# Kernel optimization log

Hardware: AMD Instinct MI355X
Metric: run time of the kernel (lower is better)

Reference implementation:

```python
import jax, jax.numpy as jnp
import numpy as np

B, C, IMG, P = 16, 3, 224, 16
HP = IMG // P          # 14
NP = HP * HP           # 196 patches
PD = C * P * P         # 768 patch_dim
DIM, OUT = 768, 1024
DI, NS, DC, DTR = 2 * DIM, 16, 4, 48  # mamba: d_inner, d_state, d_conv, dt_rank
NL = 2


def _ln(x, g, b, eps=1e-5):
    m = x.mean(-1, keepdims=True)
    v = ((x - m) ** 2).mean(-1, keepdims=True)
    return (x - m) / jnp.sqrt(v + eps) * g + b


def _gelu(x):
    return jax.nn.gelu(x, approximate=False)


def _mamba_block(x, in_w, in_b, conv_w, conv_b, xproj_w, dt_w, dt_b, Alog, D, out_w, out_b):
    # x: [B, L, DIM]
    Bb, L, _ = x.shape
    xr = x @ in_w + in_b                      # [B, L, 2*DI]
    xi, res = jnp.split(xr, 2, axis=-1)
    # causal depthwise conv1d over L
    xp = jnp.pad(xi, ((0, 0), (DC - 1, 0), (0, 0)))
    xc = conv_b + sum(xp[:, k:k + L, :] * conv_w[:, k] for k in range(DC))
    xi = jax.nn.silu(xc)
    dbc = xi @ xproj_w                        # [B, L, DTR + 2*NS]
    delta = jax.nn.softplus(dbc[..., :DTR] @ dt_w + dt_b)   # [B, L, DI]
    Bm = dbc[..., DTR:DTR + NS]               # [B, L, NS]
    Cm = dbc[..., DTR + NS:]                  # [B, L, NS]
    A = -jnp.exp(Alog)                        # [DI, NS]
    dA = jnp.exp(delta[..., None] * A)                       # [B, L, DI, NS]
    dBu = delta[..., None] * Bm[:, :, None, :] * xi[..., None]

    def step(h, inp):
        dA_t, dBu_t, C_t = inp
        h = dA_t * h + dBu_t                  # [B, DI, NS]
        y = jnp.einsum('bdn,bn->bd', h, C_t)
        return h, y

    h0 = jnp.zeros((Bb, DI, NS), x.dtype)
    _, ys = jax.lax.scan(step, h0, (dA.transpose(1, 0, 2, 3),
                                    dBu.transpose(1, 0, 2, 3),
                                    Cm.transpose(1, 0, 2)))
    y = ys.transpose(1, 0, 2) + D * xi        # [B, L, DI]
    y = y * jax.nn.silu(res)
    return y @ out_w + out_b


def setup_inputs() -> dict:
    key = jax.random.key(0)
    ks = iter(jax.random.split(key, 40))

    def rn(shape, s=0.02):
        return jax.random.normal(next(ks), shape, jnp.float32) * s

    inp = {
        'img': jax.random.normal(next(ks), (B, C, IMG, IMG), jnp.float32),
        'sa_w': rn((1, 2, 7, 7), 0.1),
        'pe_w': rn((PD, DIM)), 'pe_b': jnp.zeros((DIM,), jnp.float32),
        'pos_emb': rn((1, NP, DIM), 1.0),
        'm_in_w': rn((NL, DIM, 2 * DI)), 'm_in_b': jnp.zeros((NL, 2 * DI), jnp.float32),
        'm_conv_w': rn((NL, DI, DC), 0.1), 'm_conv_b': jnp.zeros((NL, DI), jnp.float32),
        'm_xproj_w': rn((NL, DI, DTR + 2 * NS)),
        'm_dt_w': rn((NL, DTR, DI)), 'm_dt_b': rn((NL, DI), 0.01),
        'm_Alog': jnp.tile(jnp.log(jnp.arange(1, NS + 1, dtype=jnp.float32))[None, None, :], (NL, DI, 1)),
        'm_D': jnp.ones((NL, DI), jnp.float32),
        'm_out_w': rn((NL, DI, DIM)), 'm_out_b': jnp.zeros((NL, DIM), jnp.float32),
        'em_w': rn((DIM, OUT)), 'em_b': jnp.zeros((OUT,), jnp.float32),
        'em_g': jnp.ones((OUT,), jnp.float32), 'em_bt': jnp.zeros((OUT,), jnp.float32),
        'att_w': rn((OUT, OUT)), 'att_b': jnp.zeros((OUT,), jnp.float32),
        'att_g': jnp.ones((OUT,), jnp.float32), 'att_bt': jnp.zeros((OUT,), jnp.float32),
        'lat_g': jnp.ones((OUT,), jnp.float32), 'lat_bt': jnp.zeros((OUT,), jnp.float32),
    }
    return inp


def reference(img, sa_w, pe_w, pe_b, pos_emb,
              m_in_w, m_in_b, m_conv_w, m_conv_b, m_xproj_w,
              m_dt_w, m_dt_b, m_Alog, m_D, m_out_w, m_out_b,
              em_w, em_b, em_g, em_bt, att_w, att_b, att_g, att_bt,
              lat_g, lat_bt):
    # spatial attention gate
    avg = img.mean(axis=1, keepdims=True)
    mx = img.max(axis=1, keepdims=True)
    a = jnp.concatenate([avg, mx], axis=1)                    # [B,2,H,W]
    a = jax.lax.conv_general_dilated(a, sa_w, (1, 1), [(3, 3), (3, 3)],
                                     dimension_numbers=('NCHW', 'OIHW', 'NCHW'))
    img = img * jax.nn.sigmoid(a)
    # patchify: b c (h p1)(w p2) -> b (h w) (p1 p2 c)
    x = img.reshape(B, C, HP, P, HP, P).transpose(0, 2, 4, 3, 5, 1).reshape(B, NP, PD)
    x = x @ pe_w + pe_b                                       # [B, NP, DIM]
    x = x + pos_emb[:, :NP]
    for i in range(NL):
        x = _mamba_block(x, m_in_w[i], m_in_b[i], m_conv_w[i], m_conv_b[i],
                         m_xproj_w[i], m_dt_w[i], m_dt_b[i], m_Alog[i], m_D[i],
                         m_out_w[i], m_out_b[i])
    y = _gelu(_ln(x @ em_w + em_b, em_g, em_bt))              # [B, NP, OUT]
    z = jax.nn.softmax(_gelu(_ln(y @ att_w + att_b, att_g, att_bt)), axis=1)
    pooled = (y * z).sum(axis=1)                              # [B, OUT]
    return _ln(pooled, lat_g, lat_bt)
```

## Files before the change

### kernel.cpp

```cpp
#include <hip/hip_runtime.h>
#include <math.h>

static constexpr int NB = 16;
static constexpr int NC = 3;
static constexpr int IM = 224;
static constexpr int IMP = IM * IM;
static constexpr int HPq = 14;
static constexpr int NPq = 196;
static constexpr int OUTq = 1024;
static constexpr int DIq = 1536;
static constexpr int ROWS = NB * NPq;
static constexpr int MPAD = 3200;

typedef __bf16 bf8_t __attribute__((ext_vector_type(8)));
typedef float f4_t __attribute__((ext_vector_type(4)));
typedef unsigned short us8 __attribute__((ext_vector_type(8)));
typedef const __attribute__((address_space(1))) unsigned int cgu32;
typedef __attribute__((address_space(3))) unsigned int lu32;

__device__ inline unsigned short f2bf(float x) {
    unsigned u = __builtin_bit_cast(unsigned, x);
    unsigned r = (u + 0x7FFFu + ((u >> 16) & 1u)) >> 16;
    return (unsigned short)r;
}
__device__ inline float bf2f(unsigned short v) {
    return __builtin_bit_cast(float, (unsigned)v << 16);
}
__device__ inline float fast_sig(float x) {
    return __builtin_amdgcn_rcpf(1.f + __expf(-x));
}
__device__ inline float fast_softplus(float v) {
    return fmaxf(v, 0.f) + __logf(1.f + __expf(-fabsf(v)));
}

template<int CTRL>
__device__ inline float dpp_add(float x) {
    int v = __builtin_amdgcn_update_dpp(0, __builtin_bit_cast(int, x), CTRL, 0xF, 0xF, true);
    return x + __builtin_bit_cast(float, v);
}

__global__ __launch_bounds__(256) void k_avgmax(const float* __restrict__ img, float* __restrict__ am) {
    int idx = blockIdx.x * 256 + threadIdx.x;
    if (idx >= NB * IMP / 4) return;
    int p4 = (idx % (IMP / 4)) * 4, b = idx / (IMP / 4);
    const float* ib = img + (size_t)b * NC * IMP + p4;
    float4 c0 = *(const float4*)ib;
    float4 c1 = *(const float4*)(ib + IMP);
    float4 c2 = *(const float4*)(ib + 2 * IMP);
    float4 av, mx;
    av.x = (c0.x + c1.x + c2.x) * (1.f / 3.f); mx.x = fmaxf(c0.x, fmaxf(c1.x, c2.x));
    av.y = (c0.y + c1.y + c2.y) * (1.f / 3.f); mx.y = fmaxf(c0.y, fmaxf(c1.y, c2.y));
    av.z = (c0.z + c1.z + c2.z) * (1.f / 3.f); mx.z = fmaxf(c0.z, fmaxf(c1.z, c2.z));
    av.w = (c0.w + c1.w + c2.w) * (1.f / 3.f); mx.w = fmaxf(c0.w, fmaxf(c1.w, c2.w));
    *(float4*)(am + (size_t)(b * 2 + 0) * IMP + p4) = av;
    *(float4*)(am + (size_t)(b * 2 + 1) * IMP + p4) = mx;
}

__global__ __launch_bounds__(256) void k_gatepatch(const float* __restrict__ img, const float* __restrict__ am,
                                                   const float* __restrict__ saw, unsigned short* __restrict__ G) {
    int quad = blockIdx.x * 256 + threadIdx.x;
    if (quad >= NB * IMP / 4) return;
    int pq = quad % (IMP / 4), b = quad / (IMP / 4);
    int x0 = (pq % 56) * 4;
    int y = pq / 56;
    float acc0 = 0.f, acc1 = 0.f, acc2 = 0.f, acc3 = 0.f;
    const bool lok = (x0 >= 4), rok = (x0 <= IM - 8);
    #pragma unroll
    for (int ci = 0; ci < 2; ci++) {
        const float* amc = am + (size_t)(b * 2 + ci) * IMP;
        const float* wc = saw + ci * 49;
        #pragma unroll
        for (int kh = 0; kh < 7; kh++) {
            int yy = y + kh - 3;
            if (yy < 0 || yy >= IM) continue;
            const float* rowp = amc + yy * IM;
            float4 lv = lok ? *(const float4*)(rowp + x0 - 4) : make_float4(0.f, 0.f, 0.f, 0.f);
            float4 mv = *(const float4*)(rowp + x0);
            float4 rv = rok ? *(const float4*)(rowp + x0 + 4) : make_float4(0.f, 0.f, 0.f, 0.f);
            float f[12] = {lv.x, lv.y, lv.z, lv.w, mv.x, mv.y, mv.z, mv.w, rv.x, rv.y, rv.z, rv.w};
            #pragma unroll
            for (int kw = 0; kw < 7; kw++) {
                float w = wc[kh * 7 + kw];
                acc0 = fmaf(w, f[kw + 1], acc0);
                acc1 = fmaf(w, f[kw + 2], acc1);
                acc2 = fmaf(w, f[kw + 3], acc2);
                acc3 = fmaf(w, f[kw + 4], acc3);
            }
        }
    }
    float s0 = fast_sig(acc0), s1 = fast_sig(acc1), s2 = fast_sig(acc2), s3 = fast_sig(acc3);
    const float* ib = img + (size_t)b * NC * IMP + y * IM + x0;
    float4 c0 = *(const float4*)ib;
    float4 c1 = *(const float4*)(ib + IMP);
    float4 c2 = *(const float4*)(ib + 2 * IMP);
    int hy = y >> 4, py = y & 15, hx = x0 >> 4, px0 = x0 & 15;
    size_t base = ((size_t)(b * NPq + hy * HPq + hx) * 768) + (size_t)(py * 16 + px0) * 3;
    ushort4 o0, o1, o2;
    o0.x = f2bf(c0.x * s0); o0.y = f2bf(c1.x * s0); o0.z = f2bf(c2.x * s0);
    o0.w = f2bf(c0.y * s1);
    o1.x = f2bf(c1.y * s1); o1.y = f2bf(c2.y * s1);
    o1.z = f2bf(c0.z * s2); o1.w = f2bf(c1.z * s2);
    o2.x = f2bf(c2.z * s2);
    o2.y = f2bf(c0.w * s3); o2.z = f2bf(c1.w * s3); o2.w = f2bf(c2.w * s3);
    *(ushort4*)(G + base + 0) = o0;
    *(ushort4*)(G + base + 4) = o1;
    *(ushort4*)(G + base + 8) = o2;
}

__global__ __launch_bounds__(256) void k_transpose_all(const float* pe_w, const float* in_w, const float* ot_w,
                                                       const float* em_w, const float* at_w,
                                                       unsigned short* wpe, unsigned short* win0, unsigned short* win1,
                                                       unsigned short* wot0, unsigned short* wot1,
                                                       unsigned short* wem, unsigned short* wat) {
    int bid = blockIdx.x;
    const float* W; unsigned short* Wt; int K, N, local;
    if (bid < 576)       { W = pe_w; Wt = wpe; K = 768; N = 768; local = bid; }
    else if (bid < 2880) { W = in_w; Wt = win0; K = 768; N = 3072; local = bid - 576; }
    else if (bid < 5184) { W = in_w + (size_t)768 * 3072; Wt = win1; K = 768; N = 3072; local = bid - 2880; }
    else if (bid < 6336) { W = ot_w; Wt = wot0; K = 1536; N = 768; local = bid - 5184; }
    else if (bid < 7488) { W = ot_w + (size_t)1536 * 768; Wt = wot1; K = 1536; N = 768; local = bid - 6336; }
    else if (bid < 8256) { W = em_w; Wt = wem; K = 768; N = 1024; local = bid - 7488; }
    else                 { W = at_w; Wt = wat; K = 1024; N = 1024; local = bid - 8256; }
    int gx = N / 32;
    int n0 = (local % gx) * 32, k0 = (local / gx) * 32;
    __shared__ float t[32][33];
    int c = threadIdx.x & 31, r8 = threadIdx.x >> 5;
    #pragma unroll
    for (int i = 0; i < 4; i++) {
        int r = r8 + i * 8;
        t[r][c] = W[(size_t)(k0 + r) * N + n0 + c];
    }
    __syncthreads();
    #pragma unroll
    for (int i = 0; i < 4; i++) {
        int r = r8 + i * 8;
        Wt[(size_t)(n0 + r) * K + k0 + c] = f2bf(t[c][r]);
    }
}

enum { EPI_NONE = 0, EPI_POSEMB = 1 };

template<int EPI, bool CBF>
__global__ __launch_bounds__(256) void k_gemm_bf(const unsigned short* __restrict__ A,
                                                 const unsigned short* __restrict__ Wt,
                                                 const float* __restrict__ bias,
                                                 void* __restrict__ Cv, int ldc,
                                                 int M, int N, int K,
                                                 const float* __restrict__ extra) {
    constexpr int BM = 128, BN = 64;
    __shared__ __align__(16) unsigned short As[2][BM * 64];
    __shared__ __align__(16) unsigned short Bs[2][BN * 64];
    const int bm = blockIdx.y * BM, bn = blockIdx.x * BN;
    const int tid = threadIdx.x;
    const int lane = tid & 63;
    const int wbase = tid & ~63;
    const int wr = ((tid >> 7) & 1) * 64;
    const int wc = ((tid >> 6) & 1) * 32;
    const int lr = lane & 15, lq = lane >> 4;

    f4_t acc[4][2] = {};

    auto stage = [&](int buf, int k0) {
        #pragma unroll
        for (int i = 0; i < 4; i++) {
            int gid2 = i * 256 + tid;
            int r = gid2 >> 3, g = gid2 & 7;
            const unsigned short* src = A + (size_t)(bm + r) * K + k0 + ((g ^ (r & 7)) * 8);
            __builtin_amdgcn_global_load_lds((cgu32*)src,
                (lu32*)&As[buf][(i * 256 + wbase) * 8], 16, 0, 0);
        }
        #pragma unroll
        for (int i = 0; i < 2; i++) {
            int gid2 = i * 256 + tid;
            int r = gid2 >> 3, g = gid2 & 7;
            const unsigned short* src = Wt + (size_t)(bn + r) * K + k0 + ((g ^ (r & 7)) * 8);
            __builtin_amdgcn_global_load_lds((cgu32*)src,
                (lu32*)&Bs[buf][(i * 256 + wbase) * 8], 16, 0, 0);
        }
    };

    stage(0, 0);
    __syncthreads();
    int cur = 0;
    for (int k0 = 0; k0 < K; k0 += 64) {
        if (k0 + 64 < K) stage(cur ^ 1, k0 + 64);
        #pragma unroll
        for (int h = 0; h < 2; h++) {
            bf8_t af[4], bfr[2];
            #pragma unroll
            for (int mb = 0; mb < 4; mb++) {
                int row = wr + mb * 16 + lr;
                int g = h * 4 + lq;
                af[mb] = *(const bf8_t*)&As[cur][row * 64 + ((g ^ (row & 7)) * 8)];
            }
            #pragma unroll
            for (int nb = 0; nb < 2; nb++) {
                int rn = wc + nb * 16 + lr;
                int g = h * 4 + lq;
                bfr[nb] = *(const bf8_t*)&Bs[cur][rn * 64 + ((g ^ (rn & 7)) * 8)];
            }
            #pragma unroll
            for (int mb = 0; mb < 4; mb++)
                #pragma unroll
                for (int nb = 0; nb < 2; nb++)
                    acc[mb][nb] = __builtin_amdgcn_mfma_f32_16x16x32_bf16(af[mb], bfr[nb], acc[mb][nb], 0, 0, 0);
        }
        __syncthreads();
        cur ^= 1;
    }

    #pragma unroll
    for (int mb = 0; mb < 4; mb++) {
        #pragma unroll
        for (int nb = 0; nb < 2; nb++) {
            int col = bn + wc + nb * 16 + lr;
            #pragma unroll
            for (int q = 0; q < 4; q++) {
                int row = bm + wr + mb * 16 + lq * 4 + q;
                if (row < M) {
                    float v = acc[mb][nb][q];
                    if (bias) v += bias[col];
                    if (EPI == EPI_POSEMB) v += extra[(size_t)(row % NPq) * N + col];
                    if (CBF) ((unsigned short*)Cv)[(size_t)row * ldc + col] = f2bf(v);
                    else     ((float*)Cv)[(size_t)row * ldc + col] = v;
                }
            }
        }
    }
}

__global__ __launch_bounds__(256) void k_gemm_bf2(const unsigned short* __restrict__ A,
                                                  const unsigned short* __restrict__ Wt,
                                                  const float* __restrict__ bias,
                                                  unsigned short* __restrict__ xr2,
                                                  unsigned short* __restrict__ sres,
                                                  int M, int K) {
    constexpr int BM = 128;
    __shared__ __align__(16) unsigned short As[BM * 64];
    __shared__ __align__(16) unsigned short Bs[BM * 64];
    const int bm = blockIdx.y * BM, bn = blockIdx.x * BM;
    const int tid = threadIdx.x;
    const int lane = tid & 63;
    const int wbase = tid & ~63;
    const int wid = tid >> 6;
    const int wr = (wid >> 1) * 64;
    const int wc = (wid & 1) * 64;
    const int lr = lane & 15, lq = lane >> 4;

    f4_t acc[4][4] = {};

    for (int k0 = 0; k0 < K; k0 += 64) {
        #pragma unroll
        for (int i = 0; i < 4; i++) {
            int gid2 = i * 256 + tid;
            int r = gid2 >> 3, g = gid2 & 7;
            const unsigned short* srcA = A + (size_t)(bm + r) * K + k0 + ((g ^ (r & 7)) * 8);
            __builtin_amdgcn_global_load_lds((cgu32*)srcA,
                (lu32*)&As[(i * 256 + wbase) * 8], 16, 0, 0);
            const unsigned short* srcB = Wt + (size_t)(bn + r) * K + k0 + ((g ^ (r & 7)) * 8);
            __builtin_amdgcn_global_load_lds((cgu32*)srcB,
                (lu32*)&Bs[(i * 256 + wbase) * 8], 16, 0, 0);
        }
        __syncthreads();
        #pragma unroll
        for (int h = 0; h < 2; h++) {
            bf8_t af[4], bfr[4];
            #pragma unroll
            for (int mb = 0; mb < 4; mb++) {
                int row = wr + mb * 16 + lr;
                int g = h * 4 + lq;
                af[mb] = *(const bf8_t*)&As[row * 64 + ((g ^ (row & 7)) * 8)];
            }
            #pragma unroll
            for (int nb = 0; nb < 4; nb++) {
                int rn = wc + nb * 16 + lr;
                int g = h * 4 + lq;
                bfr[nb] = *(const bf8_t*)&Bs[rn * 64 + ((g ^ (rn & 7)) * 8)];
            }
            #pragma unroll
            for (int mb = 0; mb < 4; mb++)
                #pragma unroll
                for (int nb = 0; nb < 4; nb++)
                    acc[mb][nb] = __builtin_amdgcn_mfma_f32_16x16x32_bf16(af[mb], bfr[nb], acc[mb][nb], 0, 0, 0);
        }
        __syncthreads();
    }

    #pragma unroll
    for (int mb = 0; mb < 4; mb++) {
        #pragma unroll
        for (int nb = 0; nb < 4; nb++) {
            int col = bn + wc + nb * 16 + lr;
            float bv = bias[col];
            #pragma unroll
            for (int q = 0; q < 4; q++) {
                int row = bm + wr + mb * 16 + lq * 4 + q;
                if (row < M) {
                    float v = acc[mb][nb][q] + bv;
                    if (col < DIq) xr2[(size_t)row * DIq + col] = f2bf(v);
                    else           sres[(size_t)row * DIq + (col - DIq)] = f2bf(v * fast_sig(v));
                }
            }
        }
    }
}

static constexpr int XP_KS = 8;
static constexpr int XP_KC = 1536 / XP_KS;

__global__ __launch_bounds__(256) void k_xproj_part(const unsigned short* __restrict__ xi2b,
                                                    const float* __restrict__ W,
                                                    float* __restrict__ part) {
    __shared__ float As[32][65];
    __shared__ __align__(16) float Bs[64][80];
    int m0 = blockIdx.x * 32;
    int kc0 = blockIdx.y * XP_KC;
    int tid = threadIdx.x;
    int row = tid >> 3, cg = (tid & 7) * 10;
    float acc[10] = {};
    for (int k0 = 0; k0 < XP_KC; k0 += 64) {
        {
            int r = tid >> 3, c8 = (tid & 7) * 8;
            us8 v = *(const us8*)(xi2b + (size_t)(m0 + r) * 1536 + kc0 + k0 + c8);
            #pragma unroll
            for (int j = 0; j < 8; j++) As[r][c8 + j] = bf2f(v[j]);
        }
        #pragma unroll
        for (int i = 0; i < 5; i++) {
            int id = tid + i * 256;
            int r = id / 20, c4 = (id % 20) * 4;
            *(float4*)&Bs[r][c4] = *(const float4*)(W + (size_t)(kc0 + k0 + r) * 80 + c4);
        }
        __syncthreads();
        #pragma unroll
        for (int kk = 0; kk < 64; kk++) {
            float a = As[row][kk];
            #pragma unroll
            for (int j = 0; j < 10; j++)
                acc[j] = fmaf(a, Bs[kk][cg + j], acc[j]);
        }
        __syncthreads();
    }
    float* p = part + ((size_t)blockIdx.y * ROWS + m0 + row) * 80 + cg;
    #pragma unroll
    for (int j = 0; j < 10; j++) p[j] = acc[j];
}

static constexpr int DT_RPB = 4;
__global__ __launch_bounds__(384) void k_dtred(const float* __restrict__ part, const float* __restrict__ W,
                                               const float* __restrict__ bias, float* __restrict__ de,
                                               float* __restrict__ dbc) {
    int r0 = blockIdx.x * DT_RPB;
    int tid = threadIdx.x;
    __shared__ float ds[DT_RPB][80];
    if (tid < DT_RPB * 80) {
        int row = tid / 80, col = tid % 80;
        const int S = ROWS * 80;
        const float* p = part + (size_t)(r0 + row) * 80 + col;
        float s = 0.f;
        #pragma unroll
        for (int k = 0; k < XP_KS; k++) s += p[(size_t)k * S];
        ds[row][col] = s;
        if (col >= 48) dbc[(size_t)(r0 + row) * 80 + col] = s;
    }
    __syncthreads();
    int j = tid * 4;
    float4 b = *(const float4*)(bias + j);
    float4 a0 = b, a1 = b, a2 = b, a3 = b;
    for (int k = 0; k < 48; k++) {
        float4 w = *(const float4*)(W + (size_t)k * 1536 + j);
        float d0 = ds[0][k], d1 = ds[1][k], d2 = ds[2][k], d3 = ds[3][k];
        a0.x = fmaf(d0, w.x, a0.x); a0.y = fmaf(d0, w.y, a0.y); a0.z = fmaf(d0, w.z, a0.z); a0.w = fmaf(d0, w.w, a0.w);
        a1.x = fmaf(d1, w.x, a1.x); a1.y = fmaf(d1, w.y, a1.y); a1.z = fmaf(d1, w.z, a1.z); a1.w = fmaf(d1, w.w, a1.w);
        a2.x = fmaf(d2, w.x, a2.x); a2.y = fmaf(d2, w.y, a2.y); a2.z = fmaf(d2, w.z, a2.z); a2.w = fmaf(d2, w.w, a2.w);
        a3.x = fmaf(d3, w.x, a3.x); a3.y = fmaf(d3, w.y, a3.y); a3.z = fmaf(d3, w.z, a3.z); a3.w = fmaf(d3, w.w, a3.w);
    }
    float4 o;
    o.x = fast_softplus(a0.x); o.y = fast_softplus(a0.y); o.z = fast_softplus(a0.z); o.w = fast_softplus(a0.w);
    *(float4*)(de + (size_t)(r0 + 0) * 1536 + j) = o;
    o.x = fast_softplus(a1.x); o.y = fast_softplus(a1.y); o.z = fast_softplus(a1.z); o.w = fast_softplus(a1.w);
    *(float4*)(de + (size_t)(r0 + 1) * 1536 + j) = o;
    o.x = fast_softplus(a2.x); o.y = fast_softplus(a2.y); o.z = fast_softplus(a2.z); o.w = fast_softplus(a2.w);
    *(float4*)(de + (size_t)(r0 + 2) * 1536 + j) = o;
    o.x = fast_softplus(a3.x); o.y = fast_softplus(a3.y); o.z = fast_softplus(a3.z); o.w = fast_softplus(a3.w);
    *(float4*)(de + (size_t)(r0 + 3) * 1536 + j) = o;
}

__global__ __launch_bounds__(256) void k_conv_silu(const unsigned short* __restrict__ xr2, const float* __restrict__ cw,
                                                   const float* __restrict__ cb, unsigned short* __restrict__ xi2b) {
    int idx4 = blockIdx.x * 256 + threadIdx.x;
    if (idx4 >= ROWS * DIq / 4) return;
    int d4 = (idx4 % (DIq / 4)) * 4;
    int bt = idx4 / (DIq / 4);
    int t = bt % NPq, b = bt / NPq;
    const unsigned short* base = xr2 + (size_t)b * NPq * DIq + d4;
    float4 s = *(const float4*)(cb + d4);
    float4 w0 = *(const float4*)(cw + (d4 + 0) * 4);
    float4 w1 = *(const float4*)(cw + (d4 + 1) * 4);
    float4 w2 = *(const float4*)(cw + (d4 + 2) * 4);
    float4 w3 = *(const float4*)(cw + (d4 + 3) * 4);
    if (t >= 3) {
        ushort4 v = *(const ushort4*)(base + (size_t)(t - 3) * DIq);
        s.x = fmaf(bf2f(v.x), w0.x, s.x); s.y = fmaf(bf2f(v.y), w1.x, s.y);
        s.z = fmaf(bf2f(v.z), w2.x, s.z); s.w = fmaf(bf2f(v.w), w3.x, s.w);
    }
    if (t >= 2) {
        ushort4 v = *(const ushort4*)(base + (size_t)(t - 2) * DIq);
        s.x = fmaf(bf2f(v.x), w0.y, s.x); s.y = fmaf(bf2f(v.y), w1.y, s.y);
        s.z = fmaf(bf2f(v.z), w2.y, s.z); s.w = fmaf(bf2f(v.w), w3.y, s.w);
    }
    if (t >= 1) {
        ushort4 v = *(const ushort4*)(base + (size_t)(t - 1) * DIq);
        s.x = fmaf(bf2f(v.x), w0.z, s.x); s.y = fmaf(bf2f(v.y), w1.z, s.y);
        s.z = fmaf(bf2f(v.z), w2.z, s.z); s.w = fmaf(bf2f(v.w), w3.z, s.w);
    }
    {
        ushort4 v = *(const ushort4*)(base + (size_t)t * DIq);
        s.x = fmaf(bf2f(v.x), w0.w, s.x); s.y = fmaf(bf2f(v.y), w1.w, s.y);
        s.z = fmaf(bf2f(v.z), w2.w, s.z); s.w = fmaf(bf2f(v.w), w3.w, s.w);
    }
    ushort4 xo;
    xo.x = f2bf(s.x * fast_sig(s.x)); xo.y = f2bf(s.y * fast_sig(s.y));
    xo.z = f2bf(s.z * fast_sig(s.z)); xo.w = f2bf(s.w * fast_sig(s.w));
    *(ushort4*)(xi2b + (size_t)bt * DIq + d4) = xo;
}

static constexpr int STB = 28;

__global__ __launch_bounds__(256) void k_scan(const float* __restrict__ delta, const unsigned short* __restrict__ xi2b,
                                              const float* __restrict__ dbc, const unsigned short* __restrict__ sresb,
                                              const float* __restrict__ Alog, const float* __restrict__ Dv,
                                              unsigned short* __restrict__ ys) {
    const int b = blockIdx.x;
    const int d0 = blockIdx.y * 32;
    const int tid = threadIdx.x;
    const int dl = tid >> 3;
    const int np = tid & 7;
    const int d = d0 + dl;
    const float A0 = -__expf(Alog[d * 16 + np]);
    const float A1 = -__expf(Alog[d * 16 + np + 8]);
    const float Dd = Dv[d];
    const int tr = tid >> 5;
    const int dls = tid & 31;

    __shared__ float2 sdu[2][STB][32];
    __shared__ float sbc[2][STB][32];

    const float* gde = delta + ((size_t)b * NPq + tr) * DIq + d0 + dls;
    const unsigned short* gu  = xi2b  + ((size_t)b * NPq + tr) * DIq + d0 + dls;
    const unsigned short* gsr = sresb + ((size_t)b * NPq + tr) * DIq + d0 + dls;
    const float* gbc = dbc + ((size_t)b * NPq + tr) * 80 + 48 + dls;
    unsigned short* gy = ys + (size_t)b * NPq * DIq + d;

    float rde[4], rbc[4];
    unsigned short ruu[4], rss[4];

    auto stageLoad = [&](int c) {
        const int t0 = c * STB;
        #pragma unroll
        for (int j = 0; j < 3; j++) {
            int off = (t0 + 8 * j) * DIq;
            rde[j] = gde[off];
            ruu[j] = gu[off];
            rss[j] = gsr[off];
            rbc[j] = gbc[(t0 + 8 * j) * 80];
        }
        if (tid < 128) {
            int off = (t0 + 24) * DIq;
            rde[3] = gde[off];
            ruu[3] = gu[off];
            rss[3] = gsr[off];
            rbc[3] = gbc[(t0 + 24) * 80];
        }
    };
    auto stageWrite = [&](int buf) {
        const int pi = (dls & 7) * 4 + (dls >> 3);
        #pragma unroll
        for (int j = 0; j < 3; j++) {
            int t = tr + 8 * j;
            unsigned pk = ((unsigned)ruu[j] << 16) | rss[j];
            sdu[buf][t][dls] = make_float2(rde[j], __builtin_bit_cast(float, pk));
            sbc[buf][t][pi] = rbc[j];
        }
        if (tid < 128) {
            int t = tr + 24;
            unsigned pk = ((unsigned)ruu[3] << 16) | rss[3];
            sdu[buf][t][dls] = make_float2(rde[3], __builtin_bit_cast(float, pk));
            sbc[buf][t][pi] = rbc[3];
        }
    };

    stageLoad(0);
    stageWrite(0);
    __syncthreads();

    float h0 = 0.f, h1 = 0.f;
    int cur = 0;
    for (int c = 0; c < 7; c++) {
        if (c < 6) stageLoad(c + 1);
        #pragma unroll 4
        for (int t = 0; t < STB; t++) {
            float2 duv = sdu[cur][t][dl];
            float4 bc = *(const float4*)&sbc[cur][t][np * 4];
            unsigned bits = __builtin_bit_cast(unsigned, duv.y);
            float u  = __builtin_bit_cast(float, bits & 0xFFFF0000u);
            float sr = __builtin_bit_cast(float, bits << 16);
            float a0 = __expf(duv.x * A0), a1 = __expf(duv.x * A1);
            float deu = duv.x * u;
            h0 = fmaf(a0, h0, deu * bc.x);
            h1 = fmaf(a1, h1, deu * bc.y);
            float p = fmaf(h1, bc.w, h0 * bc.z);
            p = dpp_add<0xB1>(p);
            p = dpp_add<0x4E>(p);
            p = dpp_add<0x141>(p);
            if (np == 0) gy[(size_t)(c * STB + t) * DIq] = f2bf(fmaf(Dd, u, p) * sr);
        }
        if (c < 6) stageWrite(cur ^ 1);
        __syncthreads();
        cur ^= 1;
    }
}

template<bool OBF>
__global__ __launch_bounds__(256) void k_ln_gelu(const float* __restrict__ in, const float* __restrict__ g,
                                                 const float* __restrict__ bt, void* __restrict__ outv) {
    int row = blockIdx.x;
    const float* x = in + (size_t)row * OUTq;
    float4 v = ((const float4*)x)[threadIdx.x];
    float s = v.x + v.y + v.z + v.w;
    float ss = v.x * v.x + v.y * v.y + v.z * v.z + v.w * v.w;
    #pragma unroll
    for (int off = 32; off >= 1; off >>= 1) { s += __shfl_down(s, off); ss += __shfl_down(ss, off); }
    __shared__ float sh[10];
    int wid = threadIdx.x >> 6, lid = threadIdx.x & 63;
    if (lid == 0) { sh[wid] = s; sh[4 + wid] = ss; }
    __syncthreads();
    if (threadIdx.x == 0) {
        float S = sh[0] + sh[1] + sh[2] + sh[3], SS = sh[4] + sh[5] + sh[6] + sh[7];
        float m = S * (1.f / OUTq);
        float var = SS * (1.f / OUTq) - m * m;
        sh[8] = m; sh[9] = rsqrtf(var + 1e-5f);
    }
    __syncthreads();
    float m = sh[8], rst = sh[9];
    float4 gv = ((const float4*)g)[threadIdx.x];
    float4 bv = ((const float4*)bt)[threadIdx.x];
    float4 o;
    float y0 = (v.x - m) * rst * gv.x + bv.x; o.x = 0.5f * y0 * (1.f + erff(y0 * 0.70710678118f));
    float y1 = (v.y - m) * rst * gv.y + bv.y; o.y = 0.5f * y1 * (1.f + erff(y1 * 0.70710678118f));
    float y2 = (v.z - m) * rst * gv.z + bv.z; o.z = 0.5f * y2 * (1.f + erff(y2 * 0.70710678118f));
    float y3 = (v.w - m) * rst * gv.w + bv.w; o.w = 0.5f * y3 * (1.f + erff(y3 * 0.70710678118f));
    if (OBF) {
        ushort4 o4;
        o4.x = f2bf(o.x); o4.y = f2bf(o.y); o4.z = f2bf(o.z); o4.w = f2bf(o.w);
        ((ushort4*)((unsigned short*)outv + (size_t)row * OUTq))[threadIdx.x] = o4;
    } else {
        ((float4*)((float*)outv + (size_t)row * OUTq))[threadIdx.x] = o;
    }
}

__global__ __launch_bounds__(256) void k_softpool(const float* __restrict__ gm, const unsigned short* __restrict__ ym,
                                                  float* __restrict__ pooled) {
    int b = blockIdx.y;
    int jl = threadIdx.x & 63;
    int j = blockIdx.x * 64 + jl;
    int tc = threadIdx.x >> 6;
    const float* gb = gm + (size_t)b * NPq * OUTq + j;
    const unsigned short* yb = ym + (size_t)b * NPq * OUTq + j;
    int t0 = tc * 49;
    float m = -1e30f, s = 0.f, ps = 0.f;
    for (int t = t0; t < t0 + 49; t++) {
        float g = gb[(size_t)t * OUTq];
        float y = bf2f(yb[(size_t)t * OUTq]);
        float mn = fmaxf(m, g);
        float sc = __expf(m - mn);
        float e = __expf(g - mn);
        s = fmaf(s, sc, e);
        ps = fmaf(ps, sc, y * e);
        m = mn;
    }
    __shared__ float sm[4][64], ssum[4][64], sps[4][64];
    sm[tc][jl] = m; ssum[tc][jl] = s; sps[tc][jl] = ps;
    __syncthreads();
    if (tc == 0) {
        float m0 = sm[0][jl], m1 = sm[1][jl], m2 = sm[2][jl], m3 = sm[3][jl];
        float mt = fmaxf(fmaxf(m0, m1), fmaxf(m2, m3));
        float e0 = __expf(m0 - mt), e1 = __expf(m1 - mt);
        float e2 = __expf(m2 - mt), e3 = __expf(m3 - mt);
        float st = ssum[0][jl] * e0 + ssum[1][jl] * e1 + ssum[2][jl] * e2 + ssum[3][jl] * e3;
        float pt = sps[0][jl] * e0 + sps[1][jl] * e1 + sps[2][jl] * e2 + sps[3][jl] * e3;
        pooled[b * OUTq + j] = pt / st;
    }
}

__global__ __launch_bounds__(256) void k_final_ln(const float* __restrict__ p, const float* __restrict__ g,
                                                  const float* __restrict__ bt, float* __restrict__ out) {
    int row = blockIdx.x;
    const float* x = p + (size_t)row * OUTq;
    float4 v = ((const float4*)x)[threadIdx.x];
    float s = v.x + v.y + v.z + v.w;
    float ss = v.x * v.x + v.y * v.y + v.z * v.z + v.w * v.w;
    #pragma unroll
    for (int off = 32; off >= 1; off >>= 1) { s += __shfl_down(s, off); ss += __shfl_down(ss, off); }
    __shared__ float sh[10];
    int wid = threadIdx.x >> 6, lid = threadIdx.x & 63;
    if (lid == 0) { sh[wid] = s; sh[4 + wid] = ss; }
    __syncthreads();
    if (threadIdx.x == 0) {
        float S = sh[0] + sh[1] + sh[2] + sh[3], SS = sh[4] + sh[5] + sh[6] + sh[7];
        float m = S * (1.f / OUTq);
        float var = SS * (1.f / OUTq) - m * m;
        sh[8] = m; sh[9] = rsqrtf(var + 1e-5f);
    }
    __syncthreads();
    float m = sh[8], rst = sh[9];
    float4 gv = ((const float4*)g)[threadIdx.x];
    float4 bv = ((const float4*)bt)[threadIdx.x];
    float4 o;
    o.x = (v.x - m) * rst * gv.x + bv.x;
    o.y = (v.y - m) * rst * gv.y + bv.y;
    o.z = (v.z - m) * rst * gv.z + bv.z;
    o.w = (v.w - m) * rst * gv.w + bv.w;
    ((float4*)(out + (size_t)row * OUTq))[threadIdx.x] = o;
}

extern "C" void kernel_launch(void* const* d_in, const int* in_sizes, int n_in,
                              void* d_out, int out_size, void* d_ws, size_t ws_size,
                              hipStream_t stream) {
    const float* img   = (const float*)d_in[0];
    const float* sa_w  = (const float*)d_in[1];
    const float* pe_w  = (const float*)d_in[2];
    const float* pe_b  = (const float*)d_in[3];
    const float* pos   = (const float*)d_in[4];
    const float* in_w  = (const float*)d_in[5];
    const float* in_b  = (const float*)d_in[6];
    const float* cv_w  = (const float*)d_in[7];
    const float* cv_b  = (const float*)d_in[8];
    const float* xp_w  = (const float*)d_in[9];
    const float* dt_w  = (const float*)d_in[10];
    const float* dt_b  = (const float*)d_in[11];
    const float* Alog  = (const float*)d_in[12];
    const float* Dv    = (const float*)d_in[13];
    const float* ot_w  = (const float*)d_in[14];
    const float* ot_b  = (const float*)d_in[15];
    const float* em_w  = (const float*)d_in[16];
    const float* em_b  = (const float*)d_in[17];
    const float* em_g  = (const float*)d_in[18];
    const float* em_bt = (const float*)d_in[19];
    const float* at_w  = (const float*)d_in[20];
    const float* at_b  = (const float*)d_in[21];
    const float* at_g  = (const float*)d_in[22];
    const float* at_bt = (const float*)d_in[23];
    const float* la_g  = (const float*)d_in[24];
    const float* la_bt = (const float*)d_in[25];

    char* ws = (char*)d_ws;
    auto al = [](size_t x) { return (x + 255) & ~(size_t)255; };
    size_t SZ_am   = (size_t)NB * 2 * IMP * 4;
    size_t SZ_G    = (size_t)MPAD * 768 * 2;
    size_t SZ_x    = (size_t)MPAD * 768 * 2;
    size_t SZ_xr2  = (size_t)ROWS * DIq * 2;
    size_t SZ_xi2  = (size_t)ROWS * DIq * 2;
    size_t SZ_de   = (size_t)ROWS * DIq * 4;
    size_t SZ_dbc  = (size_t)ROWS * 80 * 4;
    size_t SZ_ys   = (size_t)MPAD * DIq * 2;
    size_t SZ_sres = (size_t)ROWS * DIq * 2;
    size_t SZ_yem  = (size_t)MPAD * 1024 * 2;
    size_t SZ_pool = (size_t)NB * OUTq * 4;
    size_t SZ_part = (size_t)XP_KS * ROWS * 80 * 4;

    size_t o_am   = 0;
    size_t o_G    = al(o_am + SZ_am);
    size_t o_x    = al(o_G + SZ_G);
    size_t o_xr2  = al(o_x + SZ_x);
    size_t o_xi2  = al(o_xr2 + SZ_xr2);
    size_t o_de   = al(o_xi2 + SZ_xi2);
    size_t o_dbc  = al(o_de + SZ_de);
    size_t o_ys   = al(o_dbc + SZ_dbc);
    size_t o_sres = al(o_ys + SZ_ys);
    size_t o_yem  = al(o_sres + SZ_sres);
    size_t o_pool = al(o_yem + SZ_yem);
    size_t o_part = al(o_pool + SZ_pool);

    size_t o_wpe  = al(o_part + SZ_part);
    size_t o_win0 = al(o_wpe  + (size_t)768 * 768 * 2);
    size_t o_win1 = al(o_win0 + (size_t)3072 * 768 * 2);
    size_t o_wot0 = al(o_win1 + (size_t)3072 * 768 * 2);
    size_t o_wot1 = al(o_wot0 + (size_t)768 * 1536 * 2);
    size_t o_wem  = al(o_wot1 + (size_t)768 * 1536 * 2);
    size_t o_wat  = al(o_wem  + (size_t)1024 * 768 * 2);

    float* am    = (float*)(ws + o_am);
    unsigned short* G   = (unsigned short*)(ws + o_G);
    unsigned short* x   = (unsigned short*)(ws + o_x);
    unsigned short* xr2 = (unsigned short*)(ws + o_xr2);
    unsigned short* xi2b = (unsigned short*)(ws + o_xi2);
    float* de    = (float*)(ws + o_de);
    float* dbc   = (float*)(ws + o_dbc);
    unsigned short* ys = (unsigned short*)(ws + o_ys);
    unsigned short* sresb = (unsigned short*)(ws + o_sres);
    unsigned short* yem = (unsigned short*)(ws + o_yem);
    float* pool  = (float*)(ws + o_pool);
    float* part  = (float*)(ws + o_part);
    unsigned short* wpe  = (unsigned short*)(ws + o_wpe);
    unsigned short* win0 = (unsigned short*)(ws + o_win0);
    unsigned short* win1 = (unsigned short*)(ws + o_win1);
    unsigned short* wot0 = (unsigned short*)(ws + o_wot0);
    unsigned short* wot1 = (unsigned short*)(ws + o_wot1);
    unsigned short* wem  = (unsigned short*)(ws + o_wem);
    unsigned short* wat  = (unsigned short*)(ws + o_wat);
    float* t1  = (float*)(ws + o_de);
    float* t2  = (float*)(ws + o_xr2);
    float* gat = (float*)(ws + o_ys);

    k_transpose_all<<<9280, 256, 0, stream>>>(pe_w, in_w, ot_w, em_w, at_w,
                                              wpe, win0, win1, wot0, wot1, wem, wat);

    int nq = NB * IMP / 4;
    k_avgmax<<<(nq + 255) / 256, 256, 0, stream>>>(img, am);
    k_gatepatch<<<(nq + 255) / 256, 256, 0, stream>>>(img, am, sa_w, G);

    dim3 blk(256);
    k_gemm_bf<EPI_POSEMB, true><<<dim3(12, 25), blk, 0, stream>>>(G, wpe, pe_b, x, 768, ROWS, 768, 768, pos);

    for (int l = 0; l < 2; l++) {
        const unsigned short* win = l ? win1 : win0;
        const unsigned short* wot = l ? wot1 : wot0;
        k_gemm_bf2<<<dim3(24, 25), blk, 0, stream>>>(x, win, in_b + l * 3072, xr2, sresb, ROWS, 768);
        int nc4 = ROWS * DIq / 4;
        k_conv_silu<<<(nc4 + 255) / 256, 256, 0, stream>>>(xr2, cv_w + (size_t)l * DIq * 4, cv_b + l * DIq, xi2b);
        k_xproj_part<<<dim3(ROWS / 32, XP_KS), blk, 0, stream>>>(xi2b, xp_w + (size_t)l * 1536 * 80, part);
        k_dtred<<<ROWS / DT_RPB, 384, 0, stream>>>(part, dt_w + (size_t)l * 48 * 1536, dt_b + l * 1536, de, dbc);
        k_scan<<<dim3(16, 48), blk, 0, stream>>>(de, xi2b, dbc, sresb, Alog + (size_t)l * 1536 * 16,
                                                 Dv + l * 1536, ys);
        k_gemm_bf<EPI_NONE, true><<<dim3(12, 25), blk, 0, stream>>>(ys, wot, ot_b + l * 768, x, 768,
                                                                    ROWS, 768, 1536, nullptr);
    }

    k_gemm_bf<EPI_NONE, false><<<dim3(16, 25), blk, 0, stream>>>(x, wem, em_b, t1, 1024, ROWS, 1024, 768, nullptr);
    k_ln_gelu<true><<<ROWS, 256, 0, stream>>>(t1, em_g, em_bt, yem);
    k_gemm_bf<EPI_NONE, false><<<dim3(16, 25), blk, 0, stream>>>(yem, wat, at_b, t2, 1024, ROWS, 1024, 1024, nullptr);
    k_ln_gelu<false><<<ROWS, 256, 0, stream>>>(t2, at_g, at_bt, gat);
    k_softpool<<<dim3(16, NB), 256, 0, stream>>>(gat, yem, pool);
    k_final_ln<<<NB, 256, 0, stream>>>(pool, la_g, la_bt, (float*)d_out);
}
```

Measured before the change: 436.5 us.

## Run x_proj on the bf16 MFMA GEMM with a padded transposed weight

Result: faster. 422.3 us (-3.2%).

```diff
diff --git a/kernel.cpp b/kernel.cpp
--- a/kernel.cpp
+++ b/kernel.cpp
@@ -138,6 +138,17 @@
     }
 }
 
+__global__ __launch_bounds__(256) void k_xpw_t(const float* __restrict__ xp_w, unsigned short* __restrict__ xpt) {
+    int idx = blockIdx.x * 256 + threadIdx.x;
+    if (idx >= 2 * 128 * 1536) return;
+    int k = idx % 1536;
+    int n = (idx / 1536) % 128;
+    int l = idx / (1536 * 128);
+    unsigned short v = 0;
+    if (n < 80) v = f2bf(xp_w[(size_t)l * 1536 * 80 + (size_t)k * 80 + n]);
+    xpt[idx] = v;
+}
+
 enum { EPI_NONE = 0, EPI_POSEMB = 1 };
 
 template<int EPI, bool CBF>
@@ -305,63 +316,15 @@
     }
 }
 
-static constexpr int XP_KS = 8;
-static constexpr int XP_KC = 1536 / XP_KS;
-
-__global__ __launch_bounds__(256) void k_xproj_part(const unsigned short* __restrict__ xi2b,
-                                                    const float* __restrict__ W,
-                                                    float* __restrict__ part) {
-    __shared__ float As[32][65];
-    __shared__ __align__(16) float Bs[64][80];
-    int m0 = blockIdx.x * 32;
-    int kc0 = blockIdx.y * XP_KC;
-    int tid = threadIdx.x;
-    int row = tid >> 3, cg = (tid & 7) * 10;
-    float acc[10] = {};
-    for (int k0 = 0; k0 < XP_KC; k0 += 64) {
-        {
-            int r = tid >> 3, c8 = (tid & 7) * 8;
-            us8 v = *(const us8*)(xi2b + (size_t)(m0 + r) * 1536 + kc0 + k0 + c8);
-            #pragma unroll
-            for (int j = 0; j < 8; j++) As[r][c8 + j] = bf2f(v[j]);
-        }
-        #pragma unroll
-        for (int i = 0; i < 5; i++) {
-            int id = tid + i * 256;
-            int r = id / 20, c4 = (id % 20) * 4;
-            *(float4*)&Bs[r][c4] = *(const float4*)(W + (size_t)(kc0 + k0 + r) * 80 + c4);
-        }
-        __syncthreads();
-        #pragma unroll
-        for (int kk = 0; kk < 64; kk++) {
-            float a = As[row][kk];
-            #pragma unroll
-            for (int j = 0; j < 10; j++)
-                acc[j] = fmaf(a, Bs[kk][cg + j], acc[j]);
-        }
-        __syncthreads();
-    }
-    float* p = part + ((size_t)blockIdx.y * ROWS + m0 + row) * 80 + cg;
-    #pragma unroll
-    for (int j = 0; j < 10; j++) p[j] = acc[j];
-}
-
 static constexpr int DT_RPB = 4;
-__global__ __launch_bounds__(384) void k_dtred(const float* __restrict__ part, const float* __restrict__ W,
-                                               const float* __restrict__ bias, float* __restrict__ de,
-                                               float* __restrict__ dbc) {
+__global__ __launch_bounds__(384) void k_dtred(const float* __restrict__ dbc128, const float* __restrict__ W,
+                                               const float* __restrict__ bias, float* __restrict__ de) {
     int r0 = blockIdx.x * DT_RPB;
     int tid = threadIdx.x;
-    __shared__ float ds[DT_RPB][80];
-    if (tid < DT_RPB * 80) {
-        int row = tid / 80, col = tid % 80;
-        const int S = ROWS * 80;
-        const float* p = part + (size_t)(r0 + row) * 80 + col;
-        float s = 0.f;
-        #pragma unroll
-        for (int k = 0; k < XP_KS; k++) s += p[(size_t)k * S];
-        ds[row][col] = s;
-        if (col >= 48) dbc[(size_t)(r0 + row) * 80 + col] = s;
+    __shared__ float ds[DT_RPB][48];
+    if (tid < DT_RPB * 48) {
+        int row = tid / 48, col = tid % 48;
+        ds[row][col] = dbc128[(size_t)(r0 + row) * 128 + col];
     }
     __syncthreads();
     int j = tid * 4;
@@ -428,7 +391,7 @@
 static constexpr int STB = 28;
 
 __global__ __launch_bounds__(256) void k_scan(const float* __restrict__ delta, const unsigned short* __restrict__ xi2b,
-                                              const float* __restrict__ dbc, const unsigned short* __restrict__ sresb,
+                                              const float* __restrict__ dbc128, const unsigned short* __restrict__ sresb,
                                               const float* __restrict__ Alog, const float* __restrict__ Dv,
                                               unsigned short* __restrict__ ys) {
     const int b = blockIdx.x;
@@ -437,8 +400,8 @@
     const int dl = tid >> 3;
     const int np = tid & 7;
     const int d = d0 + dl;
-    const float A0 = -__expf(Alog[d * 16 + np]);
-    const float A1 = -__expf(Alog[d * 16 + np + 8]);
+    const float A0p = -__expf(Alog[d * 16 + np]) * 1.44269504089f;
+    const float A1p = -__expf(Alog[d * 16 + np + 8]) * 1.44269504089f;
     const float Dd = Dv[d];
     const int tr = tid >> 5;
     const int dls = tid & 31;
@@ -449,7 +412,7 @@
     const float* gde = delta + ((size_t)b * NPq + tr) * DIq + d0 + dls;
     const unsigned short* gu  = xi2b  + ((size_t)b * NPq + tr) * DIq + d0 + dls;
     const unsigned short* gsr = sresb + ((size_t)b * NPq + tr) * DIq + d0 + dls;
-    const float* gbc = dbc + ((size_t)b * NPq + tr) * 80 + 48 + dls;
+    const float* gbc = dbc128 + ((size_t)b * NPq + tr) * 128 + 48 + dls;
     unsigned short* gy = ys + (size_t)b * NPq * DIq + d;
 
     float rde[4], rbc[4];
@@ -463,14 +426,14 @@
             rde[j] = gde[off];
             ruu[j] = gu[off];
             rss[j] = gsr[off];
-            rbc[j] = gbc[(t0 + 8 * j) * 80];
+            rbc[j] = gbc[(t0 + 8 * j) * 128];
         }
         if (tid < 128) {
             int off = (t0 + 24) * DIq;
             rde[3] = gde[off];
             ruu[3] = gu[off];
             rss[3] = gsr[off];
-            rbc[3] = gbc[(t0 + 24) * 80];
+            rbc[3] = gbc[(t0 + 24) * 128];
         }
     };
     auto stageWrite = [&](int buf) {
@@ -505,7 +468,7 @@
             unsigned bits = __builtin_bit_cast(unsigned, duv.y);
             float u  = __builtin_bit_cast(float, bits & 0xFFFF0000u);
             float sr = __builtin_bit_cast(float, bits << 16);
-            float a0 = __expf(duv.x * A0), a1 = __expf(duv.x * A1);
+            float a0 = exp2f(duv.x * A0p), a1 = exp2f(duv.x * A1p);
             float deu = duv.x * u;
             h0 = fmaf(a0, h0, deu * bc.x);
             h1 = fmaf(a1, h1, deu * bc.y);
@@ -662,12 +625,11 @@
     size_t SZ_xr2  = (size_t)ROWS * DIq * 2;
     size_t SZ_xi2  = (size_t)ROWS * DIq * 2;
     size_t SZ_de   = (size_t)ROWS * DIq * 4;
-    size_t SZ_dbc  = (size_t)ROWS * 80 * 4;
+    size_t SZ_dbc  = (size_t)MPAD * 128 * 4;
     size_t SZ_ys   = (size_t)MPAD * DIq * 2;
     size_t SZ_sres = (size_t)ROWS * DIq * 2;
     size_t SZ_yem  = (size_t)MPAD * 1024 * 2;
     size_t SZ_pool = (size_t)NB * OUTq * 4;
-    size_t SZ_part = (size_t)XP_KS * ROWS * 80 * 4;
 
     size_t o_am   = 0;
     size_t o_G    = al(o_am + SZ_am);
@@ -680,15 +642,15 @@
     size_t o_sres = al(o_ys + SZ_ys);
     size_t o_yem  = al(o_sres + SZ_sres);
     size_t o_pool = al(o_yem + SZ_yem);
-    size_t o_part = al(o_pool + SZ_pool);
-
-    size_t o_wpe  = al(o_part + SZ_part);
+
+    size_t o_wpe  = al(o_pool + SZ_pool);
     size_t o_win0 = al(o_wpe  + (size_t)768 * 768 * 2);
     size_t o_win1 = al(o_win0 + (size_t)3072 * 768 * 2);
     size_t o_wot0 = al(o_win1 + (size_t)3072 * 768 * 2);
     size_t o_wot1 = al(o_wot0 + (size_t)768 * 1536 * 2);
     size_t o_wem  = al(o_wot1 + (size_t)768 * 1536 * 2);
     size_t o_wat  = al(o_wem  + (size_t)1024 * 768 * 2);
+    size_t o_xpt  = al(o_wat  + (size_t)1024 * 1024 * 2);
 
     float* am    = (float*)(ws + o_am);
     unsigned short* G   = (unsigned short*)(ws + o_G);
@@ -696,12 +658,11 @@
     unsigned short* xr2 = (unsigned short*)(ws + o_xr2);
     unsigned short* xi2b = (unsigned short*)(ws + o_xi2);
     float* de    = (float*)(ws + o_de);
-    float* dbc   = (float*)(ws + o_dbc);
+    float* dbc128 = (float*)(ws + o_dbc);
     unsigned short* ys = (unsigned short*)(ws + o_ys);
     unsigned short* sresb = (unsigned short*)(ws + o_sres);
     unsigned short* yem = (unsigned short*)(ws + o_yem);
     float* pool  = (float*)(ws + o_pool);
-    float* part  = (float*)(ws + o_part);
     unsigned short* wpe  = (unsigned short*)(ws + o_wpe);
     unsigned short* win0 = (unsigned short*)(ws + o_win0);
     unsigned short* win1 = (unsigned short*)(ws + o_win1);
@@ -709,12 +670,14 @@
     unsigned short* wot1 = (unsigned short*)(ws + o_wot1);
     unsigned short* wem  = (unsigned short*)(ws + o_wem);
     unsigned short* wat  = (unsigned short*)(ws + o_wat);
+    unsigned short* xpt  = (unsigned short*)(ws + o_xpt);
     float* t1  = (float*)(ws + o_de);
     float* t2  = (float*)(ws + o_xr2);
     float* gat = (float*)(ws + o_ys);
 
     k_transpose_all<<<9280, 256, 0, stream>>>(pe_w, in_w, ot_w, em_w, at_w,
                                               wpe, win0, win1, wot0, wot1, wem, wat);
+    k_xpw_t<<<(2 * 128 * 1536 + 255) / 256, 256, 0, stream>>>(xp_w, xpt);
 
     int nq = NB * IMP / 4;
     k_avgmax<<<(nq + 255) / 256, 256, 0, stream>>>(img, am);
@@ -729,9 +692,10 @@
         k_gemm_bf2<<<dim3(24, 25), blk, 0, stream>>>(x, win, in_b + l * 3072, xr2, sresb, ROWS, 768);
         int nc4 = ROWS * DIq / 4;
         k_conv_silu<<<(nc4 + 255) / 256, 256, 0, stream>>>(xr2, cv_w + (size_t)l * DIq * 4, cv_b + l * DIq, xi2b);
-        k_xproj_part<<<dim3(ROWS / 32, XP_KS), blk, 0, stream>>>(xi2b, xp_w + (size_t)l * 1536 * 80, part);
-        k_dtred<<<ROWS / DT_RPB, 384, 0, stream>>>(part, dt_w + (size_t)l * 48 * 1536, dt_b + l * 1536, de, dbc);
-        k_scan<<<dim3(16, 48), blk, 0, stream>>>(de, xi2b, dbc, sresb, Alog + (size_t)l * 1536 * 16,
+        k_gemm_bf<EPI_NONE, false><<<dim3(2, 25), blk, 0, stream>>>(xi2b, xpt + (size_t)l * 128 * 1536,
+                                                                    nullptr, dbc128, 128, ROWS, 128, 1536, nullptr);
+        k_dtred<<<ROWS / DT_RPB, 384, 0, stream>>>(dbc128, dt_w + (size_t)l * 48 * 1536, dt_b + l * 1536, de);
+        k_scan<<<dim3(16, 48), blk, 0, stream>>>(de, xi2b, dbc128, sresb, Alog + (size_t)l * 1536 * 16,
                                                  Dv + l * 1536, ys);
         k_gemm_bf<EPI_NONE, true><<<dim3(12, 25), blk, 0, stream>>>(ys, wot, ot_b + l * 768, x, 768,
                                                                     ROWS, 768, 1536, nullptr);
```
